# Kernel tuning notes

Hardware: AMD Instinct MI355X
Metric: run time of the kernel (lower is better)

The kernel has to match this reference:

```python
import jax, jax.numpy as jnp
import numpy as np

N, E, IN, HID, HEADS, OUT, G = 30000, 480000, 256, 64, 8, 128, 512
NEG_SLOPE = 0.2


def setup_inputs() -> dict:
    key = jax.random.key(0)
    ks = jax.random.split(key, 20)
    def nrm(k, shape, scale=0.05):
        return jax.random.normal(k, shape, dtype=jnp.float32) * scale
    inp = {
        'x': jax.random.normal(ks[0], (N, IN), dtype=jnp.float32),
        'edge_index': jax.random.randint(ks[1], (2, E), 0, N, dtype=jnp.int32),
        'batch': jnp.sort(jax.random.randint(ks[2], (N,), 0, G, dtype=jnp.int32)),
        # conv1: in=IN, out=HID, heads=HEADS (concat)
        'W1': nrm(ks[3], (IN, HEADS * HID)),
        'a_src1': nrm(ks[4], (HEADS, HID)),
        'a_dst1': nrm(ks[5], (HEADS, HID)),
        'b1': jnp.zeros((HEADS * HID,), jnp.float32),
        # conv2: in=HEADS*HID, out=HID, heads=HEADS (concat)
        'W2': nrm(ks[6], (HEADS * HID, HEADS * HID)),
        'a_src2': nrm(ks[7], (HEADS, HID)),
        'a_dst2': nrm(ks[8], (HEADS, HID)),
        'b2': jnp.zeros((HEADS * HID,), jnp.float32),
        # conv3: in=HEADS*HID, out=HID, heads=1
        'W3': nrm(ks[9], (HEADS * HID, HID)),
        'a_src3': nrm(ks[10], (1, HID)),
        'a_dst3': nrm(ks[11], (1, HID)),
        'b3': jnp.zeros((HID,), jnp.float32),
        # fc
        'Wfc': nrm(ks[12], (HID, OUT)),
        'bfc': jnp.zeros((OUT,), jnp.float32),
    }
    return inp


def gat_conv(x, W, a_src, a_dst, b, src, dst, heads, ch):
    # x: [N, in] -> h: [N, heads, ch]
    h = (x @ W).reshape(N, heads, ch)
    alpha_s = jnp.einsum('nhc,hc->nh', h, a_src)  # [N,H]
    alpha_d = jnp.einsum('nhc,hc->nh', h, a_dst)
    e = jax.nn.leaky_relu(alpha_s[src] + alpha_d[dst], NEG_SLOPE)  # [E',H]
    # segment softmax over incoming edges of each dst node
    e = e - jax.ops.segment_max(e, dst, num_segments=N)[dst]
    e = jnp.exp(e)
    alpha = e / jax.ops.segment_sum(e, dst, num_segments=N)[dst]
    msg = h[src] * alpha[:, :, None]                   # [E',H,C]
    out = jax.ops.segment_sum(msg, dst, num_segments=N)  # [N,H,C]
    return out.reshape(N, heads * ch) + b


def reference(x, edge_index, batch, W1, a_src1, a_dst1, b1, W2, a_src2, a_dst2, b2,
              W3, a_src3, a_dst3, b3, Wfc, bfc):
    # PyG GATConv adds self-loops
    loops = jnp.arange(N, dtype=edge_index.dtype)
    src = jnp.concatenate([edge_index[0], loops])
    dst = jnp.concatenate([edge_index[1], loops])

    h = jax.nn.elu(gat_conv(x, W1, a_src1, a_dst1, b1, src, dst, HEADS, HID))
    h = jax.nn.elu(gat_conv(h, W2, a_src2, a_dst2, b2, src, dst, HEADS, HID))
    h = jax.nn.elu(gat_conv(h, W3, a_src3, a_dst3, b3, src, dst, 1, HID))

    # global mean pool over graphs
    sums = jax.ops.segment_sum(h, batch, num_segments=G)          # [G,HID]
    cnt = jax.ops.segment_sum(jnp.ones((N,), h.dtype), batch, num_segments=G)
    pooled = sums / jnp.maximum(cnt, 1.0)[:, None]
    # dropout(p=0.5) is identity in eval mode
    return pooled @ Wfc + bfc  # [G, OUT]
```

## Files before the change

### kernel.cpp

```cpp
#include <hip/hip_runtime.h>
#include <hip/hip_fp16.h>
#include <math.h>

#define N_NODES 30000
#define N_EDGES 480000
#define N_EDGES_SL (N_EDGES + N_NODES)
#define CSRC_CAP (N_EDGES + 4 * N_NODES)
#define DIM_IN 256
#define F1 512
#define HEADS 8
#define NGRAPH 512
#define NEG 0.2f
#define MB_TILES 235
#define NB_SCAN 118

typedef __attribute__((ext_vector_type(8))) short short8;
typedef __attribute__((ext_vector_type(8))) _Float16 half8;
typedef __attribute__((ext_vector_type(4))) float f32x4;

__device__ __forceinline__ float lrelu(float x) { return fmaxf(x, NEG * x); }
__device__ __forceinline__ float elu_(float x) { return x > 0.f ? x : __expf(x) - 1.f; }

__device__ __forceinline__ void glds16(const unsigned short* g, unsigned short* l) {
    __builtin_amdgcn_global_load_lds(
        (const __attribute__((address_space(1))) unsigned int*)g,
        (__attribute__((address_space(3))) unsigned int*)l, 16, 0, 0);
}

__device__ __forceinline__ int plen_of(int deg) { return (deg + 4) & ~3; }

__global__ __launch_bounds__(256) void k_bsum(const int* __restrict__ deg,
                                              int* __restrict__ bsum) {
    int i = blockIdx.x * 256 + threadIdx.x;
    int v = (i < N_NODES) ? plen_of(deg[i]) : 0;
#pragma unroll
    for (int off = 1; off < 64; off <<= 1) v += __shfl_xor(v, off);
    __shared__ int ws[4];
    if ((threadIdx.x & 63) == 0) ws[threadIdx.x >> 6] = v;
    __syncthreads();
    if (threadIdx.x == 0) bsum[blockIdx.x] = ws[0] + ws[1] + ws[2] + ws[3];
}

__global__ __launch_bounds__(128) void k_bscan(const int* __restrict__ bsum,
                                               int* __restrict__ bbase,
                                               int* __restrict__ offsN) {
    __shared__ int p[128];
    int t = threadIdx.x;
    int v = (t < NB_SCAN) ? bsum[t] : 0;
    p[t] = v;
    __syncthreads();
    for (int off = 1; off < 128; off <<= 1) {
        int x = (t >= off) ? p[t - off] : 0;
        __syncthreads();
        p[t] += x;
        __syncthreads();
    }
    if (t < NB_SCAN) bbase[t] = p[t] - v;
    if (t == 127) *offsN = p[127];
}

__global__ __launch_bounds__(256) void k_offs(const int* __restrict__ deg,
                                              const int* __restrict__ bbase,
                                              int* __restrict__ offs,
                                              int* __restrict__ cursor,
                                              unsigned short* __restrict__ csrc) {
    int b = blockIdx.x, t = threadIdx.x;
    int i = b * 256 + t;
    int d1 = 0, v = 0;
    if (i < N_NODES) { d1 = deg[i] + 1; v = (d1 + 3) & ~3; }
    __shared__ int p[256];
    p[t] = v;
    __syncthreads();
    for (int off = 1; off < 256; off <<= 1) {
        int x = (t >= off) ? p[t - off] : 0;
        __syncthreads();
        p[t] += x;
        __syncthreads();
    }
    if (i < N_NODES) {
        int excl = bbase[b] + p[t] - v;
        offs[i] = excl | (v - d1);
        cursor[i] = excl;
        for (int pp = excl + d1; pp < excl + v; ++pp) csrc[pp] = 0;
    }
}

__global__ void k_scatter(const int* __restrict__ ei, int* __restrict__ cursor,
                          unsigned short* __restrict__ csrc) {
    int i = blockIdx.x * blockDim.x + threadIdx.x;
    if (i >= N_EDGES_SL) return;
    int s, d;
    if (i < N_EDGES) { s = ei[i]; d = ei[N_EDGES + i]; }
    else { s = d = i - N_EDGES; }
    int p = atomicAdd(&cursor[d], 1);
    csrc[p] = (unsigned short)s;
}

__device__ __forceinline__ void d_packA(int t, const float* __restrict__ A,
                                        unsigned short* __restrict__ out,
                                        int M, int K) {
    int KB = K >> 5;
    int k8 = t & 3;
    int ml = (t >> 2) & 127;
    int tmp = t >> 9;
    int kb = tmp % KB;
    int mb = tmp / KB;
    int m = mb * 128 + ml;
    int k0 = kb * 32 + k8 * 8;
    float v[8] = {0.f, 0.f, 0.f, 0.f, 0.f, 0.f, 0.f, 0.f};
    if (m < M) {
        float4 p0 = *(const float4*)(A + (size_t)m * K + k0);
        float4 p1 = *(const float4*)(A + (size_t)m * K + k0 + 4);
        v[0] = p0.x; v[1] = p0.y; v[2] = p0.z; v[3] = p0.w;
        v[4] = p1.x; v[5] = p1.y; v[6] = p1.z; v[7] = p1.w;
    }
    unsigned short h[8];
#pragma unroll
    for (int j = 0; j < 8; ++j) h[j] = __half_as_ushort(__float2half(v[j]));
    *(short8*)(out + (size_t)t * 8) = *(short8*)h;
}

__device__ __forceinline__ void d_packW(int t, const float* __restrict__ W,
                                        unsigned short* __restrict__ out,
                                        int K, int Nn, int BN, int LB) {
    int KB = K >> 5;
    int k8 = t & 3;
    int tmp = t >> 2;
    int nl = tmp & (BN - 1);
    int tmp2 = tmp >> LB;
    int kb = tmp2 % KB;
    int nb = tmp2 / KB;
    int n = nb * BN + nl;
    int k0 = kb * 32 + k8 * 8;
    unsigned short h[8];
#pragma unroll
    for (int j = 0; j < 8; ++j)
        h[j] = __half_as_ushort(__float2half(W[(size_t)(k0 + j) * Nn + n]));
    *(short8*)(out + (size_t)t * 8) = *(short8*)h;
}

#define PB_A 3760
#define PB_W1 64
#define PB_W2 128
#define PB_W3 16
#define PB_B 118
#define PB_CNT 1875
__global__ __launch_bounds__(256) void k_packall(
        const float* __restrict__ x, const float* __restrict__ W1,
        const float* __restrict__ W2, const float* __restrict__ W3,
        const int* __restrict__ batch, const int* __restrict__ ei,
        unsigned short* __restrict__ Ah,
        unsigned short* __restrict__ Wh1, unsigned short* __restrict__ Wh2,
        unsigned short* __restrict__ Wh3, int* __restrict__ gstart,
        int* __restrict__ deg) {
    int b = blockIdx.x, tid = threadIdx.x;
    if (b < PB_A) {
        d_packA(b * 256 + tid, x, Ah, N_NODES, DIM_IN);
    } else if (b < PB_A + PB_W1) {
        d_packW((b - PB_A) * 256 + tid, W1, Wh1, DIM_IN, F1, 128, 7);
    } else if (b < PB_A + PB_W1 + PB_W2) {
        d_packW((b - PB_A - PB_W1) * 256 + tid, W2, Wh2, F1, F1, 128, 7);
    } else if (b < PB_A + PB_W1 + PB_W2 + PB_W3) {
        d_packW((b - PB_A - PB_W1 - PB_W2) * 256 + tid, W3, Wh3, F1, 64, 64, 6);
    } else if (b < PB_A + PB_W1 + PB_W2 + PB_W3 + PB_B) {
        int bb = b - (PB_A + PB_W1 + PB_W2 + PB_W3);
        int i = bb * 256 + tid;
        if (i >= N_NODES) return;
        int bt = batch[i];
        int pb = (i == 0) ? -1 : batch[i - 1];
        for (int g = pb + 1; g <= bt; ++g) gstart[g] = i;
        if (i == N_NODES - 1)
            for (int g = bt + 1; g <= NGRAPH; ++g) gstart[g] = N_NODES;
    } else {
        int i = (b - (PB_A + PB_W1 + PB_W2 + PB_W3 + PB_B)) * 256 + tid;
        if (i < N_EDGES) atomicAdd(&deg[ei[N_EDGES + i]], 1);
    }
}
#define PACKALL_BLOCKS (PB_A + PB_W1 + PB_W2 + PB_W3 + PB_B + PB_CNT)

template <int KB>
__global__ __launch_bounds__(512) void k_gemm8(const unsigned short* __restrict__ Ah,
                                               const unsigned short* __restrict__ Bh,
                                               const float* __restrict__ a_src,
                                               const float* __restrict__ a_dst,
                                               __half* __restrict__ Hf,
                                               float* __restrict__ as_,
                                               float* __restrict__ ad_,
                                               int M) {
    __shared__ unsigned short sA[4096], sB[8192];
    const int tid = threadIdx.x, lane = tid & 63, wave = tid >> 6;
    const int mb = blockIdx.x, nbp = blockIdx.y;
    const int wm = (wave >> 2) * 64;
    const int wn = (wave & 3) * 64;
    const int fr = lane & 15, quad = lane >> 4;

    const unsigned short* pA = Ah + (size_t)mb * KB * 4096;
    const unsigned short* pB0 = Bh + (size_t)(2 * nbp) * KB * 4096;
    const unsigned short* pB1 = Bh + (size_t)(2 * nbp + 1) * KB * 4096;

    f32x4 acc[4][4];
#pragma unroll
    for (int i = 0; i < 4; ++i)
#pragma unroll
        for (int j = 0; j < 4; ++j) acc[i][j] = {0.f, 0.f, 0.f, 0.f};

    for (int kb = 0; kb < KB; ++kb) {
        glds16(pA + kb * 4096 + wave * 512 + lane * 8, &sA[wave * 512]);
#pragma unroll
        for (int s = 0; s < 2; ++s) {
            int idx = wave * 2 + s;
            const unsigned short* bt = (idx < 8) ? pB0 : pB1;
            int off = (idx & 7) * 512;
            glds16(bt + kb * 4096 + off + lane * 8, &sB[(idx >> 3) * 4096 + off]);
        }
        __syncthreads();

        half8 af[4], bf[4];
#pragma unroll
        for (int f = 0; f < 4; ++f) {
            int m = wm + f * 16 + fr;
            af[f] = *(const half8*)&sA[m * 32 + quad * 8];
            int n = wn + f * 16 + fr;
            bf[f] = *(const half8*)&sB[n * 32 + quad * 8];
        }
#pragma unroll
        for (int i = 0; i < 4; ++i)
#pragma unroll
            for (int j = 0; j < 4; ++j)
                acc[i][j] = __builtin_amdgcn_mfma_f32_16x16x32_f16(af[i], bf[j], acc[i][j], 0, 0, 0);
        __syncthreads();
    }
    const int head = nbp * 4 + (wave & 3);
    float avs[4], avd[4];
#pragma unroll
    for (int j = 0; j < 4; ++j) {
        avs[j] = a_src[head * 64 + j * 16 + fr];
        avd[j] = a_dst[head * 64 + j * 16 + fr];
    }
    __half* Hh = Hf + (size_t)head * N_NODES * 64;
#pragma unroll
    for (int i = 0; i < 4; ++i) {
#pragma unroll
        for (int r = 0; r < 4; ++r) {
            int row = mb * 128 + wm + i * 16 + quad * 4 + r;
            bool ok = row < M;
            float vs = 0.f, vd = 0.f;
#pragma unroll
            for (int j = 0; j < 4; ++j) {
                float c = acc[i][j][r];
                vs = fmaf(c, avs[j], vs);
                vd = fmaf(c, avd[j], vd);
                if (ok) Hh[(size_t)row * 64 + j * 16 + fr] = __float2half(c);
            }
#pragma unroll
            for (int off = 1; off < 16; off <<= 1) {
                vs += __shfl_xor(vs, off);
                vd += __shfl_xor(vd, off);
            }
            if (ok && fr == 0) {
                as_[head * N_NODES + row] = vs;
                ad_[head * N_NODES + row] = vd;
            }
        }
    }
}

template <int KB>
__global__ __launch_bounds__(256) void k_gemm1(const unsigned short* __restrict__ Ah,
                                               const unsigned short* __restrict__ Bh,
                                               const float* __restrict__ a_src,
                                               const float* __restrict__ a_dst,
                                               __half* __restrict__ C,
                                               float* __restrict__ as_,
                                               float* __restrict__ ad_,
                                               int M) {
    __shared__ unsigned short sA[4096], sB[2048];
    const int tid = threadIdx.x, lane = tid & 63, wave = tid >> 6;
    const int mb = blockIdx.x;
    const int wm = (wave >> 1) * 64;
    const int wn = (wave & 1) * 32;
    const int fr = lane & 15, quad = lane >> 4;

    const unsigned short* pA = Ah + (size_t)mb * KB * 4096;

    f32x4 acc[4][2];
#pragma unroll
    for (int i = 0; i < 4; ++i)
#pragma unroll
        for (int j = 0; j < 2; ++j) acc[i][j] = {0.f, 0.f, 0.f, 0.f};

    for (int kb = 0; kb < KB; ++kb) {
        const unsigned short* a_g = pA + kb * 4096;
        const unsigned short* b_g = Bh + kb * 2048;
#pragma unroll
        for (int s = 0; s < 2; ++s) {
            int sg = wave * 2 + s;
            glds16(a_g + sg * 512 + lane * 8, &sA[sg * 512]);
        }
        glds16(b_g + wave * 512 + lane * 8, &sB[wave * 512]);
        __syncthreads();

        half8 af[4], bf[2];
#pragma unroll
        for (int f = 0; f < 4; ++f) {
            int m = wm + f * 16 + fr;
            af[f] = *(const half8*)&sA[m * 32 + quad * 8];
        }
#pragma unroll
        for (int f = 0; f < 2; ++f) {
            int n = wn + f * 16 + fr;
            bf[f] = *(const half8*)&sB[n * 32 + quad * 8];
        }
#pragma unroll
        for (int i = 0; i < 4; ++i)
#pragma unroll
            for (int j = 0; j < 2; ++j)
                acc[i][j] = __builtin_amdgcn_mfma_f32_16x16x32_f16(af[i], bf[j], acc[i][j], 0, 0, 0);
        __syncthreads();
    }
    float avs[2], avd[2];
#pragma unroll
    for (int j = 0; j < 2; ++j) {
        avs[j] = a_src[wn + j * 16 + fr];
        avd[j] = a_dst[wn + j * 16 + fr];
    }
    float* ps = (float*)sA;
    float* pd = (float*)sB;
#pragma unroll
    for (int i = 0; i < 4; ++i) {
#pragma unroll
        for (int r = 0; r < 4; ++r) {
            int rl = wm + i * 16 + quad * 4 + r;
            int row = mb * 128 + rl;
            bool ok = row < M;
            float vs = 0.f, vd = 0.f;
#pragma unroll
            for (int j = 0; j < 2; ++j) {
                float c = acc[i][j][r];
                vs = fmaf(c, avs[j], vs);
                vd = fmaf(c, avd[j], vd);
                if (ok) C[(size_t)row * 64 + wn + j * 16 + fr] = __float2half(c);
            }
#pragma unroll
            for (int off = 1; off < 16; off <<= 1) {
                vs += __shfl_xor(vs, off);
                vd += __shfl_xor(vd, off);
            }
            if (fr == 0) {
                ps[wave * 64 + (rl & 63)] = vs;
                pd[wave * 64 + (rl & 63)] = vd;
            }
        }
    }
    __syncthreads();
    if (tid < 128) {
        int row = mb * 128 + tid;
        if (row < M) {
            int wp = (tid >> 6) * 2;
            as_[row] = ps[wp * 64 + (tid & 63)] + ps[(wp + 1) * 64 + (tid & 63)];
            ad_[row] = pd[wp * 64 + (tid & 63)] + pd[(wp + 1) * 64 + (tid & 63)];
        }
    }
}

__device__ __forceinline__ void edge_fma(float w, uint4 u, float* a) {
    const _Float16* hp = (const _Float16*)&u;
#pragma unroll
    for (int k = 0; k < 8; ++k) a[k] = fmaf(w, (float)hp[k], a[k]);
}

__global__ __launch_bounds__(256) void k_agg8(const __half* __restrict__ Hf,
                                              const float* __restrict__ as_,
                                              const float* __restrict__ ad_,
                                              const int* __restrict__ offs,
                                              const unsigned short* __restrict__ csrc,
                                              const float* __restrict__ bias,
                                              unsigned short* __restrict__ outA) {
    const int head = blockIdx.x & 7;
    const int bg = blockIdx.x >> 3;
    const int wave = threadIdx.x >> 6, lane = threadIdx.x & 63;
    const int g = lane >> 3, cl = lane & 7;
    const unsigned coff = (unsigned)(cl * 8);
    const __half* Hh = Hf + (size_t)head * N_NODES * 64;
    const float* ash = as_ + head * N_NODES;
    const float* adh = ad_ + head * N_NODES;

    int d0 = (bg * 4 + wave) * 8;
    if (d0 >= N_NODES) return;
    int dst = d0 + g;

    float bia[8];
#pragma unroll
    for (int j = 0; j < 8; ++j) bia[j] = bias[head * 64 + cl * 8 + j];

    int raw0 = offs[dst], raw1 = offs[dst + 1];
    int beg = raw0 & ~3;
    int plen = (raw1 & ~3) - beg;
    int nreal = 4 - (raw0 & 3);
    float adv = adh[dst];
    const unsigned short* cp = csrc + beg;

    float s = 0.f;
    float a[8] = {0.f, 0.f, 0.f, 0.f, 0.f, 0.f, 0.f, 0.f};
    float b[8] = {0.f, 0.f, 0.f, 0.f, 0.f, 0.f, 0.f, 0.f};
    ushort4 idx = *(const ushort4*)cp;
    int loc = 0;
    for (; loc < plen - 4; loc += 4) {
        unsigned i0 = idx.x, i1 = idx.y, i2 = idx.z, i3 = idx.w;
        float e0 = ash[i0], e1 = ash[i1], e2 = ash[i2], e3 = ash[i3];
        uint4 u0 = *(const uint4*)(Hh + i0 * 64u + coff);
        uint4 u1 = *(const uint4*)(Hh + i1 * 64u + coff);
        uint4 u2 = *(const uint4*)(Hh + i2 * 64u + coff);
        uint4 u3 = *(const uint4*)(Hh + i3 * 64u + coff);
        idx = *(const ushort4*)(cp + loc + 4);
        float w0 = __expf(lrelu(e0 + adv));
        float w1 = __expf(lrelu(e1 + adv));
        float w2 = __expf(lrelu(e2 + adv));
        float w3 = __expf(lrelu(e3 + adv));
        s += (w0 + w1) + (w2 + w3);
        edge_fma(w0, u0, a);
        edge_fma(w1, u1, b);
        edge_fma(w2, u2, a);
        edge_fma(w3, u3, b);
    }
    {
        unsigned i0 = idx.x, i1 = idx.y, i2 = idx.z, i3 = idx.w;
        float e0 = ash[i0], e1 = ash[i1], e2 = ash[i2], e3 = ash[i3];
        uint4 u0 = *(const uint4*)(Hh + i0 * 64u + coff);
        uint4 u1 = *(const uint4*)(Hh + i1 * 64u + coff);
        uint4 u2 = *(const uint4*)(Hh + i2 * 64u + coff);
        uint4 u3 = *(const uint4*)(Hh + i3 * 64u + coff);
        float w0 = __expf(lrelu(e0 + adv));
        float w1 = (nreal > 1) ? __expf(lrelu(e1 + adv)) : 0.f;
        float w2 = (nreal > 2) ? __expf(lrelu(e2 + adv)) : 0.f;
        float w3 = (nreal > 3) ? __expf(lrelu(e3 + adv)) : 0.f;
        s += (w0 + w1) + (w2 + w3);
        edge_fma(w0, u0, a);
        edge_fma(w1, u1, b);
        edge_fma(w2, u2, a);
        edge_fma(w3, u3, b);
    }
    float inv = 1.f / s;
    unsigned short h[8];
#pragma unroll
    for (int k = 0; k < 8; ++k)
        h[k] = __half_as_ushort(__float2half(elu_((a[k] + b[k]) * inv + bia[k])));
    int c0 = head * 64 + cl * 8;
    int kb = c0 >> 5, kl = c0 & 31;
    int mb = dst >> 7, ml = dst & 127;
    size_t oo = (((size_t)(mb * 16 + kb) * 128 + ml) * 32 + kl);
    *(short8*)(outA + oo) = *(short8*)h;
}

__global__ __launch_bounds__(256) void k_agg1(const __half* __restrict__ Hf,
                                              const float* __restrict__ as_,
                                              const float* __restrict__ ad_,
                                              const int* __restrict__ offs,
                                              const unsigned short* __restrict__ csrc,
                                              const float* __restrict__ bias,
                                              float* __restrict__ h3) {
    const int wave = threadIdx.x >> 6, lane = threadIdx.x & 63;
    const int g = lane >> 3, cl = lane & 7;
    const unsigned coff = (unsigned)(cl * 8);
    int d0 = (blockIdx.x * 4 + wave) * 8;
    if (d0 >= N_NODES) return;
    int dst = d0 + g;
    float bia[8];
#pragma unroll
    for (int j = 0; j < 8; ++j) bia[j] = bias[cl * 8 + j];

    int raw0 = offs[dst], raw1 = offs[dst + 1];
    int beg = raw0 & ~3;
    int plen = (raw1 & ~3) - beg;
    int nreal = 4 - (raw0 & 3);
    float adv = ad_[dst];
    const unsigned short* cp = csrc + beg;

    float s = 0.f;
    float a[8] = {0.f, 0.f, 0.f, 0.f, 0.f, 0.f, 0.f, 0.f};
    float b[8] = {0.f, 0.f, 0.f, 0.f, 0.f, 0.f, 0.f, 0.f};
    ushort4 idx = *(const ushort4*)cp;
    int loc = 0;
    for (; loc < plen - 4; loc += 4) {
        unsigned i0 = idx.x, i1 = idx.y, i2 = idx.z, i3 = idx.w;
        float e0 = as_[i0], e1 = as_[i1], e2 = as_[i2], e3 = as_[i3];
        uint4 u0 = *(const uint4*)(Hf + i0 * 64u + coff);
        uint4 u1 = *(const uint4*)(Hf + i1 * 64u + coff);
        uint4 u2 = *(const uint4*)(Hf + i2 * 64u + coff);
        uint4 u3 = *(const uint4*)(Hf + i3 * 64u + coff);
        idx = *(const ushort4*)(cp + loc + 4);
        float w0 = __expf(lrelu(e0 + adv));
        float w1 = __expf(lrelu(e1 + adv));
        float w2 = __expf(lrelu(e2 + adv));
        float w3 = __expf(lrelu(e3 + adv));
        s += (w0 + w1) + (w2 + w3);
        edge_fma(w0, u0, a);
        edge_fma(w1, u1, b);
        edge_fma(w2, u2, a);
        edge_fma(w3, u3, b);
    }
    {
        unsigned i0 = idx.x, i1 = idx.y, i2 = idx.z, i3 = idx.w;
        float e0 = as_[i0], e1 = as_[i1], e2 = as_[i2], e3 = as_[i3];
        uint4 u0 = *(const uint4*)(Hf + i0 * 64u + coff);
        uint4 u1 = *(const uint4*)(Hf + i1 * 64u + coff);
        uint4 u2 = *(const uint4*)(Hf + i2 * 64u + coff);
        uint4 u3 = *(const uint4*)(Hf + i3 * 64u + coff);
        float w0 = __expf(lrelu(e0 + adv));
        float w1 = (nreal > 1) ? __expf(lrelu(e1 + adv)) : 0.f;
        float w2 = (nreal > 2) ? __expf(lrelu(e2 + adv)) : 0.f;
        float w3 = (nreal > 3) ? __expf(lrelu(e3 + adv)) : 0.f;
        s += (w0 + w1) + (w2 + w3);
        edge_fma(w0, u0, a);
        edge_fma(w1, u1, b);
        edge_fma(w2, u2, a);
        edge_fma(w3, u3, b);
    }
    float inv = 1.f / s;
    float o[8];
#pragma unroll
    for (int k = 0; k < 8; ++k) o[k] = elu_((a[k] + b[k]) * inv + bia[k]);
    float* op = h3 + (size_t)dst * 64 + cl * 8;
    *(float4*)op = make_float4(o[0], o[1], o[2], o[3]);
    *(float4*)(op + 4) = make_float4(o[4], o[5], o[6], o[7]);
}

__global__ __launch_bounds__(128) void k_poolfc(const float* __restrict__ h3,
                                                const int* __restrict__ gstart,
                                                const float* __restrict__ W,
                                                const float* __restrict__ b,
                                                float* __restrict__ out) {
    int g = blockIdx.x;
    int t = threadIdx.x;
    int s0 = gstart[g], s1 = gstart[g + 1];
    int c = t & 63, half = t >> 6;
    float acc = 0.f;
    for (int r = s0 + half; r < s1; r += 2) acc += h3[(size_t)r * 64 + c];
    __shared__ float p2[128];
    __shared__ float p[64];
    p2[t] = acc;
    __syncthreads();
    if (t < 64) {
        float cntf = (float)(s1 - s0);
        p[t] = (p2[t] + p2[t + 64]) / fmaxf(cntf, 1.f);
    }
    __syncthreads();
    float o = b[t];
#pragma unroll
    for (int k = 0; k < 64; ++k) o = fmaf(p[k], W[k * 128 + t], o);
    out[g * 128 + t] = o;
}

extern "C" void kernel_launch(void* const* d_in, const int* in_sizes, int n_in,
                              void* d_out, int out_size, void* d_ws, size_t ws_size,
                              hipStream_t stream) {
    const float* x     = (const float*)d_in[0];
    const int*   ei    = (const int*)d_in[1];
    const int*   batch = (const int*)d_in[2];
    const float* W1    = (const float*)d_in[3];
    const float* as1   = (const float*)d_in[4];
    const float* ad1   = (const float*)d_in[5];
    const float* b1    = (const float*)d_in[6];
    const float* W2    = (const float*)d_in[7];
    const float* as2   = (const float*)d_in[8];
    const float* ad2   = (const float*)d_in[9];
    const float* b2    = (const float*)d_in[10];
    const float* W3    = (const float*)d_in[11];
    const float* as3   = (const float*)d_in[12];
    const float* ad3   = (const float*)d_in[13];
    const float* b3    = (const float*)d_in[14];
    const float* Wfc   = (const float*)d_in[15];
    const float* bfc   = (const float*)d_in[16];
    float* out = (float*)d_out;

    char* ws = (char*)d_ws;
    size_t off = 0;
    auto alloc = [&](size_t bytes) -> void* {
        void* p = ws + off;
        off += (bytes + 255) & ~(size_t)255;
        return p;
    };
    __half* Hf = (__half*)alloc((size_t)HEADS * N_NODES * 64 * 2);
    __half* Hf3 = (__half*)alloc((size_t)N_NODES * 64 * 2);
    float* h3 = (float*)alloc((size_t)N_NODES * 64 * 4);
    unsigned short* Ah = (unsigned short*)alloc((size_t)MB_TILES * 16 * 4096 * 2);
    unsigned short* Wh1 = (unsigned short*)alloc((size_t)131072 * 2);
    unsigned short* Wh2 = (unsigned short*)alloc((size_t)262144 * 2);
    unsigned short* Wh3 = (unsigned short*)alloc((size_t)32768 * 2);
    float* asb   = (float*)alloc((size_t)HEADS * N_NODES * 4);
    float* adb   = (float*)alloc((size_t)HEADS * N_NODES * 4);
    int*   offs  = (int*)alloc((N_NODES + 1) * 4);
    int*   deg   = (int*)alloc(N_NODES * 4);
    int*   cursor= (int*)alloc(N_NODES * 4);
    unsigned short* csrc = (unsigned short*)alloc((size_t)CSRC_CAP * 2 + 64);
    int*   bsum  = (int*)alloc(NB_SCAN * 4);
    int*   bbase = (int*)alloc(NB_SCAN * 4);
    int*   gstart= (int*)alloc((NGRAPH + 1) * 4);

    hipMemsetAsync(deg, 0, N_NODES * 4, stream);

    k_packall<<<PACKALL_BLOCKS, 256, 0, stream>>>(x, W1, W2, W3, batch, ei, Ah,
                                                  Wh1, Wh2, Wh3, gstart, deg);
    k_bsum<<<NB_SCAN, 256, 0, stream>>>(deg, bsum);
    k_bscan<<<1, 128, 0, stream>>>(bsum, bbase, offs + N_NODES);
    k_offs<<<NB_SCAN, 256, 0, stream>>>(deg, bbase, offs, cursor, csrc);
    k_scatter<<<(N_EDGES_SL + 255) / 256, 256, 0, stream>>>(ei, cursor, csrc);

    k_gemm8<8><<<dim3(MB_TILES, 2), 512, 0, stream>>>(Ah, Wh1, as1, ad1, Hf, asb, adb, N_NODES);
    k_agg8<<<938 * 8, 256, 0, stream>>>(Hf, asb, adb, offs, csrc, b1, Ah);

    k_gemm8<16><<<dim3(MB_TILES, 2), 512, 0, stream>>>(Ah, Wh2, as2, ad2, Hf, asb, adb, N_NODES);
    k_agg8<<<938 * 8, 256, 0, stream>>>(Hf, asb, adb, offs, csrc, b2, Ah);

    k_gemm1<16><<<MB_TILES, 256, 0, stream>>>(Ah, Wh3, as3, ad3, Hf3, asb, adb, N_NODES);
    k_agg1<<<940, 256, 0, stream>>>(Hf3, asb, adb, offs, csrc, b3, h3);

    k_poolfc<<<NGRAPH, 128, 0, stream>>>(h3, gstart, Wfc, bfc, out);
}
```

Measured before the change: 345.7 us.

## Sort destinations by degree per block in aggregation, use exp2 with prescaled logits

In both aggregation kernels, each block of 32 destination nodes now ranks its nodes by padded edge count in shared memory. Nodes with similar degree end up in the same wave, which cuts loop divergence among the 8 node-groups of a wave. Separately, the GEMM epilogues premultiply the attention logits by log2(e), so the per-edge exp becomes exp2f. This is exact because leaky ReLU commutes with positive scaling. The cost is two extra __syncthreads, a small O(32^2) rank step per block, and bounds guards for the tail block.

```diff
diff --git a/kernel.cpp b/kernel.cpp
--- a/kernel.cpp
+++ b/kernel.cpp
@@ -11,6 +11,7 @@
 #define HEADS 8
 #define NGRAPH 512
 #define NEG 0.2f
+#define LOG2E 1.44269504f
 #define MB_TILES 235
 #define NB_SCAN 118
 
@@ -258,8 +259,8 @@
                 vd += __shfl_xor(vd, off);
             }
             if (ok && fr == 0) {
-                as_[head * N_NODES + row] = vs;
-                ad_[head * N_NODES + row] = vd;
+                as_[head * N_NODES + row] = vs * LOG2E;
+                ad_[head * N_NODES + row] = vd * LOG2E;
             }
         }
     }
@@ -357,8 +358,8 @@
         int row = mb * 128 + tid;
         if (row < M) {
             int wp = (tid >> 6) * 2;
-            as_[row] = ps[wp * 64 + (tid & 63)] + ps[(wp + 1) * 64 + (tid & 63)];
-            ad_[row] = pd[wp * 64 + (tid & 63)] + pd[(wp + 1) * 64 + (tid & 63)];
+            as_[row] = (ps[wp * 64 + (tid & 63)] + ps[(wp + 1) * 64 + (tid & 63)]) * LOG2E;
+            ad_[row] = (pd[wp * 64 + (tid & 63)] + pd[(wp + 1) * 64 + (tid & 63)]) * LOG2E;
         }
     }
 }
@@ -378,26 +379,46 @@
                                               unsigned short* __restrict__ outA) {
     const int head = blockIdx.x & 7;
     const int bg = blockIdx.x >> 3;
-    const int wave = threadIdx.x >> 6, lane = threadIdx.x & 63;
+    const int tid = threadIdx.x;
+    const int wave = tid >> 6, lane = tid & 63;
     const int g = lane >> 3, cl = lane & 7;
     const unsigned coff = (unsigned)(cl * 8);
     const __half* Hh = Hf + (size_t)head * N_NODES * 64;
     const float* ash = as_ + head * N_NODES;
     const float* adh = ad_ + head * N_NODES;
-
-    int d0 = (bg * 4 + wave) * 8;
-    if (d0 >= N_NODES) return;
-    int dst = d0 + g;
+    const int d0b = bg * 32;
+
+    __shared__ int s_raw0[32], s_raw1[32], s_key[32], s_ord[32];
+    if (tid < 32) {
+        int d = d0b + tid;
+        int r0 = 0, r1 = 0;
+        if (d < N_NODES) { r0 = offs[d]; r1 = offs[d + 1]; }
+        s_raw0[tid] = r0;
+        s_raw1[tid] = r1;
+        s_key[tid] = (((r1 & ~3) - (r0 & ~3)) << 5) | tid;
+    }
+    __syncthreads();
+    if (tid < 32) {
+        int my = s_key[tid];
+        int rank = 0;
+#pragma unroll
+        for (int j = 0; j < 32; ++j) rank += (s_key[j] < my) ? 1 : 0;
+        s_ord[rank] = tid;
+    }
+    __syncthreads();
+
+    const int ld = s_ord[wave * 8 + g];
+    const int dst = d0b + ld;
 
     float bia[8];
 #pragma unroll
     for (int j = 0; j < 8; ++j) bia[j] = bias[head * 64 + cl * 8 + j];
 
-    int raw0 = offs[dst], raw1 = offs[dst + 1];
+    int raw0 = s_raw0[ld], raw1 = s_raw1[ld];
     int beg = raw0 & ~3;
     int plen = (raw1 & ~3) - beg;
     int nreal = 4 - (raw0 & 3);
-    float adv = adh[dst];
+    float adv = adh[min(dst, N_NODES - 1)];
     const unsigned short* cp = csrc + beg;
 
     float s = 0.f;
@@ -413,10 +434,10 @@
         uint4 u2 = *(const uint4*)(Hh + i2 * 64u + coff);
         uint4 u3 = *(const uint4*)(Hh + i3 * 64u + coff);
         idx = *(const ushort4*)(cp + loc + 4);
-        float w0 = __expf(lrelu(e0 + adv));
-        float w1 = __expf(lrelu(e1 + adv));
-        float w2 = __expf(lrelu(e2 + adv));
-        float w3 = __expf(lrelu(e3 + adv));
+        float w0 = exp2f(lrelu(e0 + adv));
+        float w1 = exp2f(lrelu(e1 + adv));
+        float w2 = exp2f(lrelu(e2 + adv));
+        float w3 = exp2f(lrelu(e3 + adv));
         s += (w0 + w1) + (w2 + w3);
         edge_fma(w0, u0, a);
         edge_fma(w1, u1, b);
@@ -430,26 +451,28 @@
         uint4 u1 = *(const uint4*)(Hh + i1 * 64u + coff);
         uint4 u2 = *(const uint4*)(Hh + i2 * 64u + coff);
         uint4 u3 = *(const uint4*)(Hh + i3 * 64u + coff);
-        float w0 = __expf(lrelu(e0 + adv));
-        float w1 = (nreal > 1) ? __expf(lrelu(e1 + adv)) : 0.f;
-        float w2 = (nreal > 2) ? __expf(lrelu(e2 + adv)) : 0.f;
-        float w3 = (nreal > 3) ? __expf(lrelu(e3 + adv)) : 0.f;
+        float w0 = exp2f(lrelu(e0 + adv));
+        float w1 = (nreal > 1) ? exp2f(lrelu(e1 + adv)) : 0.f;
+        float w2 = (nreal > 2) ? exp2f(lrelu(e2 + adv)) : 0.f;
+        float w3 = (nreal > 3) ? exp2f(lrelu(e3 + adv)) : 0.f;
         s += (w0 + w1) + (w2 + w3);
         edge_fma(w0, u0, a);
         edge_fma(w1, u1, b);
         edge_fma(w2, u2, a);
         edge_fma(w3, u3, b);
     }
-    float inv = 1.f / s;
-    unsigned short h[8];
-#pragma unroll
-    for (int k = 0; k < 8; ++k)
-        h[k] = __half_as_ushort(__float2half(elu_((a[k] + b[k]) * inv + bia[k])));
-    int c0 = head * 64 + cl * 8;
-    int kb = c0 >> 5, kl = c0 & 31;
-    int mb = dst >> 7, ml = dst & 127;
-    size_t oo = (((size_t)(mb * 16 + kb) * 128 + ml) * 32 + kl);
-    *(short8*)(outA + oo) = *(short8*)h;
+    if (dst < N_NODES) {
+        float inv = 1.f / s;
+        unsigned short h[8];
+#pragma unroll
+        for (int k = 0; k < 8; ++k)
+            h[k] = __half_as_ushort(__float2half(elu_((a[k] + b[k]) * inv + bia[k])));
+        int c0 = head * 64 + cl * 8;
+        int kb = c0 >> 5, kl = c0 & 31;
+        int mb = dst >> 7, ml = dst & 127;
+        size_t oo = (((size_t)(mb * 16 + kb) * 128 + ml) * 32 + kl);
+        *(short8*)(outA + oo) = *(short8*)h;
+    }
 }
 
 __global__ __launch_bounds__(256) void k_agg1(const __half* __restrict__ Hf,
@@ -459,21 +482,44 @@
                                               const unsigned short* __restrict__ csrc,
                                               const float* __restrict__ bias,
                                               float* __restrict__ h3) {
-    const int wave = threadIdx.x >> 6, lane = threadIdx.x & 63;
+    const int bg = blockIdx.x;
+    const int tid = threadIdx.x;
+    const int wave = tid >> 6, lane = tid & 63;
     const int g = lane >> 3, cl = lane & 7;
     const unsigned coff = (unsigned)(cl * 8);
-    int d0 = (blockIdx.x * 4 + wave) * 8;
-    if (d0 >= N_NODES) return;
-    int dst = d0 + g;
+    const int d0b = bg * 32;
+
+    __shared__ int s_raw0[32], s_raw1[32], s_key[32], s_ord[32];
+    if (tid < 32) {
+        int d = d0b + tid;
+        int r0 = 0, r1 = 0;
+        if (d < N_NODES) { r0 = offs[d]; r1 = offs[d + 1]; }
+        s_raw0[tid] = r0;
+        s_raw1[tid] = r1;
+        s_key[tid] = (((r1 & ~3) - (r0 & ~3)) << 5) | tid;
+    }
+    __syncthreads();
+    if (tid < 32) {
+        int my = s_key[tid];
+        int rank = 0;
+#pragma unroll
+        for (int j = 0; j < 32; ++j) rank += (s_key[j] < my) ? 1 : 0;
+        s_ord[rank] = tid;
+    }
+    __syncthreads();
+
+    const int ld = s_ord[wave * 8 + g];
+    const int dst = d0b + ld;
+
     float bia[8];
 #pragma unroll
     for (int j = 0; j < 8; ++j) bia[j] = bias[cl * 8 + j];
 
-    int raw0 = offs[dst], raw1 = offs[dst + 1];
+    int raw0 = s_raw0[ld], raw1 = s_raw1[ld];
     int beg = raw0 & ~3;
     int plen = (raw1 & ~3) - beg;
     int nreal = 4 - (raw0 & 3);
-    float adv = ad_[dst];
+    float adv = ad_[min(dst, N_NODES - 1)];
     const unsigned short* cp = csrc + beg;
 
     float s = 0.f;
@@ -489,10 +535,10 @@
         uint4 u2 = *(const uint4*)(Hf + i2 * 64u + coff);
         uint4 u3 = *(const uint4*)(Hf + i3 * 64u + coff);
         idx = *(const ushort4*)(cp + loc + 4);
-        float w0 = __expf(lrelu(e0 + adv));
-        float w1 = __expf(lrelu(e1 + adv));
-        float w2 = __expf(lrelu(e2 + adv));
-        float w3 = __expf(lrelu(e3 + adv));
+        float w0 = exp2f(lrelu(e0 + adv));
+        float w1 = exp2f(lrelu(e1 + adv));
+        float w2 = exp2f(lrelu(e2 + adv));
+        float w3 = exp2f(lrelu(e3 + adv));
         s += (w0 + w1) + (w2 + w3);
         edge_fma(w0, u0, a);
         edge_fma(w1, u1, b);
@@ -506,23 +552,25 @@
         uint4 u1 = *(const uint4*)(Hf + i1 * 64u + coff);
         uint4 u2 = *(const uint4*)(Hf + i2 * 64u + coff);
         uint4 u3 = *(const uint4*)(Hf + i3 * 64u + coff);
-        float w0 = __expf(lrelu(e0 + adv));
-        float w1 = (nreal > 1) ? __expf(lrelu(e1 + adv)) : 0.f;
-        float w2 = (nreal > 2) ? __expf(lrelu(e2 + adv)) : 0.f;
-        float w3 = (nreal > 3) ? __expf(lrelu(e3 + adv)) : 0.f;
+        float w0 = exp2f(lrelu(e0 + adv));
+        float w1 = (nreal > 1) ? exp2f(lrelu(e1 + adv)) : 0.f;
+        float w2 = (nreal > 2) ? exp2f(lrelu(e2 + adv)) : 0.f;
+        float w3 = (nreal > 3) ? exp2f(lrelu(e3 + adv)) : 0.f;
         s += (w0 + w1) + (w2 + w3);
         edge_fma(w0, u0, a);
         edge_fma(w1, u1, b);
         edge_fma(w2, u2, a);
         edge_fma(w3, u3, b);
     }
-    float inv = 1.f / s;
-    float o[8];
-#pragma unroll
-    for (int k = 0; k < 8; ++k) o[k] = elu_((a[k] + b[k]) * inv + bia[k]);
-    float* op = h3 + (size_t)dst * 64 + cl * 8;
-    *(float4*)op = make_float4(o[0], o[1], o[2], o[3]);
-    *(float4*)(op + 4) = make_float4(o[4], o[5], o[6], o[7]);
+    if (dst < N_NODES) {
+        float inv = 1.f / s;
+        float o[8];
+#pragma unroll
+        for (int k = 0; k < 8; ++k) o[k] = elu_((a[k] + b[k]) * inv + bia[k]);
+        float* op = h3 + (size_t)dst * 64 + cl * 8;
+        *(float4*)op = make_float4(o[0], o[1], o[2], o[3]);
+        *(float4*)(op + 4) = make_float4(o[4], o[5], o[6], o[7]);
+    }
 }
 
 __global__ __launch_bounds__(128) void k_poolfc(const float* __restrict__ h3,
@@ -613,7 +661,7 @@
     k_agg8<<<938 * 8, 256, 0, stream>>>(Hf, asb, adb, offs, csrc, b2, Ah);
 
     k_gemm1<16><<<MB_TILES, 256, 0, stream>>>(Ah, Wh3, as3, ad3, Hf3, asb, adb, N_NODES);
-    k_agg1<<<940, 256, 0, stream>>>(Hf3, asb, adb, offs, csrc, b3, h3);
+    k_agg1<<<938, 256, 0, stream>>>(Hf3, asb, adb, offs, csrc, b3, h3);
 
     k_poolfc<<<NGRAPH, 128, 0, stream>>>(h3, gstart, Wfc, bfc, out);
 }
```

Measured after the change: 348.8 us. Within noise of the previous version (+0.9%).
